# Optimization experiments

Hardware: AMD Instinct MI355X
Metric: run time of the kernel (lower is better)

The kernel has to match this reference:

```python
import jax, jax.numpy as jnp
import numpy as np

B, N, IN_FT, OUT_FT = 2, 4096, 512, 256
NEG = -9e15
EPS = 1e-12

def _prelu(x, a):
    return jnp.where(x >= 0, x, a * x)

def _normalize(x):
    n = jnp.sqrt(jnp.sum(x * x, axis=-1, keepdims=True))
    return x / jnp.maximum(n, EPS)

def _xavier(key, shape):
    fan_out, fan_in = shape
    lim = np.sqrt(6.0 / (fan_in + fan_out))
    return jax.random.uniform(key, shape, jnp.float32, -lim, lim)

def setup_inputs() -> dict:
    key = jax.random.key(0)
    ks = jax.random.split(key, 8)
    seq = jax.random.normal(ks[0], (B, N, IN_FT), jnp.float32)
    # sparse-ish random adjacency with self loops, row-normalized (typical GCN input)
    u = jax.random.uniform(ks[1], (B, N, N))
    mask = (u < 0.01).astype(jnp.float32)
    eye = jnp.eye(N, dtype=jnp.float32)[None]
    mask = jnp.maximum(mask, eye)
    adj = mask / jnp.sum(mask, axis=-1, keepdims=True)
    return {
        "seq": seq,
        "adj": adj,
        "W_fc": _xavier(ks[2], (OUT_FT, IN_FT)),
        "W_q": _xavier(ks[3], (OUT_FT, OUT_FT)),
        "W_k": _xavier(ks[4], (OUT_FT, OUT_FT)),
        "W_v1": _xavier(ks[5], (OUT_FT, OUT_FT)),
        "W_v2": _xavier(ks[6], (OUT_FT, OUT_FT)),
        "a_v": jnp.asarray(0.25, jnp.float32),    # PReLU inside to_v
        "a_act": jnp.asarray(0.25, jnp.float32),  # final PReLU self.act
        "bias": jnp.zeros((OUT_FT,), jnp.float32),
    }

def reference(seq, adj, W_fc, W_q, W_k, W_v1, W_v2, a_v, a_act, bias):
    # attn=True, training=False (dropout is identity) path of GCN.forward
    seq_fts = jnp.einsum('bnd,od->bno', seq, W_fc)            # fc (no bias)
    out = jnp.einsum('bmn,bno->bmo', adj, seq_fts)            # bmm(adj, seq_fts)
    out_q = _normalize(jnp.einsum('bno,po->bnp', out, W_q))
    out_k = _normalize(jnp.einsum('bno,po->bnp', out, W_k))
    attn_mx = jax.lax.stop_gradient(jnp.einsum('bmd,bnd->bmn', out_q, out_k))
    div_loss = jnp.mean(jnp.sum((out_q - out_k) ** 2, axis=-1))
    scores = jnp.where(adj > 0, attn_mx, NEG)
    attention = jax.nn.softmax(scores, axis=-1)               # dropout skipped (eval)
    ctx = jnp.einsum('bmn,bno->bmo', attention, out)
    h = _prelu(jnp.einsum('bno,po->bnp', ctx, W_v1), a_v)
    v = jnp.einsum('bno,po->bnp', h, W_v2)
    y = _prelu(v + bias, a_act)
    return (y, div_loss)
```

## Files before the change

kernel.cpp:

```cpp
#include <hip/hip_runtime.h>
#include <hip/hip_bf16.h>


#define NN    4096
#define ROWS  8192
#define OFT   256
#define CAP   128
#define NBLK  512
#define RPB   16
#define EPSN  1e-12f
#define MFMA(a,b,c) __builtin_amdgcn_mfma_f32_16x16x32_bf16((a),(b),(c),0,0,0)

typedef unsigned short ushort_t;
typedef unsigned char  u8;
typedef __attribute__((ext_vector_type(8))) short bf16x8;
typedef __attribute__((ext_vector_type(4))) float f32x4;
typedef __attribute__((ext_vector_type(2))) float f32x2;

#define WP_FC   0
#define WP_Q    (16384 * 8)
#define WP_K    (WP_Q + 8192 * 8)
#define WP_V1   (WP_K + 8192 * 8)
#define WP_V2   (WP_V1 + 8192 * 8)

__device__ __forceinline__ float lo_f(unsigned u) { union { unsigned i; float f; } c; c.i = u << 16;          return c.f; }
__device__ __forceinline__ float hi_f(unsigned u) { union { unsigned i; float f; } c; c.i = u & 0xFFFF0000u;  return c.f; }
__device__ __forceinline__ float bf2f(ushort_t u) { union { unsigned i; float f; } c; c.i = (unsigned)u << 16; return c.f; }
__device__ __forceinline__ ushort_t f2bf(float f) {
    union { float f; unsigned i; } c; c.f = f;
    unsigned r = c.i + 0x7FFFu + ((c.i >> 16) & 1u);
    return (ushort_t)(r >> 16);
}
__device__ __forceinline__ unsigned pack2(float a, float b) {
    return (unsigned)f2bf(a) | ((unsigned)f2bf(b) << 16);
}

template<int CTRL>
__device__ __forceinline__ float dpp_add(float x) {
    union { float f; int i; } c; c.f = x;
    int y = __builtin_amdgcn_update_dpp(c.i, c.i, CTRL, 0xF, 0xF, false);
    union { int i; float f; } r; r.i = y;
    return x + r.f;
}

__global__ __launch_bounds__(256) void k0_prep(
    const float* __restrict__ Wfc, const float* __restrict__ Wq,
    const float* __restrict__ Wk,  const float* __restrict__ Wv1,
    const float* __restrict__ Wv2, ushort_t* __restrict__ Wp)
{
    int sid = blockIdx.x * 256 + threadIdx.x;
    const float* src; int K, local; ushort_t* dst;
    if (sid < 16384) { src = Wfc; K = 512; local = sid; dst = Wp + WP_FC + (size_t)local * 8; }
    else {
        int s = sid - 16384, which = s >> 13; local = s & 8191;
        const float* ws4[4] = {Wq, Wk, Wv1, Wv2};
        src = ws4[which]; K = 256;
        dst = Wp + WP_Q + (size_t)which * 65536 + (size_t)local * 8;
    }
    int col = local & 255, k8c = local >> 8;
    const float* p = src + (size_t)col * K + k8c * 8;
    float4 x0 = *(const float4*)p, x1 = *(const float4*)(p + 4);
    uint4 o; o.x = pack2(x0.x, x0.y); o.y = pack2(x0.z, x0.w);
    o.z = pack2(x1.x, x1.y); o.w = pack2(x1.z, x1.w);
    *(uint4*)dst = o;
}

__global__ __launch_bounds__(1024, 4) void k1_extract_fc(
    const float* __restrict__ seq, const float* __restrict__ adj,
    const ushort_t* __restrict__ Wp, u8* __restrict__ regA8,
    unsigned* __restrict__ gcols, int* __restrict__ cnt)
{
    __shared__ ushort_t Astage[64 * 17 * 8];
    __shared__ ushort_t csr_c[RPB * CAP];
    __shared__ int      csr_n[RPB];

    const int tid = threadIdx.x, wave = tid >> 6, lane = tid & 63;
    const int t16 = lane & 15, kq = lane >> 4;
    const int b = blockIdx.x, r0 = b * RPB;

    {
        const float4* rowp = (const float4*)(adj + (size_t)(r0 + wave) * NN);
        float4 v[16];
#pragma unroll
        for (int t = 0; t < 16; ++t) v[t] = rowp[t * 64 + lane];
        int base = 0;
#pragma unroll
        for (int h = 0; h < 2; ++h) {
            int c = 0;
#pragma unroll
            for (int t = 0; t < 8; ++t) {
                const float4& x = v[h * 8 + t];
                c += (x.x > 0.f) + (x.y > 0.f) + (x.z > 0.f) + (x.w > 0.f);
            }
            int incl = c;
#pragma unroll
            for (int off = 1; off < 64; off <<= 1) {
                int y = __shfl_up(incl, off, 64);
                if (lane >= off) incl += y;
            }
            int p = base + incl - c;
            base += __shfl(incl, 63, 64);
#pragma unroll
            for (int t = 0; t < 8; ++t) {
                const float4& x = v[h * 8 + t];
                float f[4] = {x.x, x.y, x.z, x.w};
#pragma unroll
                for (int j = 0; j < 4; ++j)
                    if (f[j] > 0.f) {
                        if (p < CAP)
                            csr_c[wave * CAP + p] = (ushort_t)(((h * 8 + t) * 64 + lane) * 4 + j);
                        ++p;
                    }
            }
        }
        if (lane == 0) csr_n[wave] = (base < CAP) ? base : CAP;
    }
    __syncthreads();
    {
        const unsigned* cc = (const unsigned*)csr_c;
        if (tid < RPB * CAP / 2) gcols[b * (RPB * CAP / 2) + tid] = cc[tid];
        if (tid < RPB) cnt[r0 + tid] = csr_n[tid];
    }

    {
        int row = tid >> 6, seg = tid & 63;
        const float* p = seq + (size_t)(r0 + row) * 512 + seg * 8;
        float4 x0 = *(const float4*)p, x1 = *(const float4*)(p + 4);
        uint4 a;
        a.x = pack2(x0.x, x0.y); a.y = pack2(x0.z, x0.w);
        a.z = pack2(x1.x, x1.y); a.w = pack2(x1.z, x1.w);
        *(bf16x8*)(Astage + ((size_t)seg * 17 + row) * 8) = *(bf16x8*)&a;
    }
    __syncthreads();

    {
        const int col = wave * 16 + t16;
        const ushort_t* Wm = Wp + WP_FC;
        f32x4 a0 = {0.f, 0.f, 0.f, 0.f};
        for (int bch = 0; bch < 4; ++bch) {
            bf16x8 wb[4];
#pragma unroll
            for (int c2 = 0; c2 < 4; ++c2) {
                int k8c = (bch * 4 + c2) * 4 + kq;
                wb[c2] = *(const bf16x8*)(Wm + ((size_t)k8c * 256 + col) * 8);
            }
#pragma unroll
            for (int c2 = 0; c2 < 4; ++c2) {
                int c = bch * 4 + c2;
                bf16x8 af = *(const bf16x8*)(Astage + ((size_t)(c * 4 + kq) * 17 + t16) * 8);
                a0 = MFMA(af, wb[c2], a0);
            }
        }
#pragma unroll
        for (int r = 0; r < 4; ++r) {
            int t8 = __builtin_amdgcn_cvt_pk_fp8_f32(a0[r] * 16.f, 0.f, 0, false);
            regA8[(size_t)(r0 + kq * 4 + r) * OFT + col] = (u8)(t8 & 0xFF);
        }
    }
}

__global__ __launch_bounds__(1024, 4) void k2_spmm_qk(
    const u8* __restrict__ regA8, unsigned* __restrict__ KO8,
    ushort_t* __restrict__ regQ, const ushort_t* __restrict__ Wp,
    const unsigned* __restrict__ gcols, const int* __restrict__ cnt,
    float* __restrict__ part)
{
    __shared__ ushort_t Astage[32 * 17 * 8];
    __shared__ ushort_t csr_c[RPB * CAP];
    __shared__ ushort_t qn_l[RPB * OFT];
    __shared__ float    red[2][RPB][8];
    __shared__ float    dlred[16];

    const int tid = threadIdx.x, wave = tid >> 6, lane = tid & 63;
    const int t16 = lane & 15, kq = lane >> 4, grp = lane >> 4;
    const int b = blockIdx.x, r0 = b * RPB;
    const size_t batb = (size_t)(b >> 8) * 4096;

    {
        unsigned* cc = (unsigned*)csr_c;
        if (tid < RPB * CAP / 2) cc[tid] = gcols[b * (RPB * CAP / 2) + tid];
    }
    __syncthreads();

    {
        const int rl = wave;
        const int n = cnt[r0 + rl];
        const u8* gA = regA8 + batb * OFT;
        float a16[16];
#pragma unroll
        for (int j = 0; j < 16; ++j) a16[j] = 0.f;
        const int nIter = (n + 3) >> 2;
        uint4 v;
        {
            int e0 = grp; int val0 = (e0 < n);
            int col0 = csr_c[rl * CAP + (val0 ? e0 : 0)];
            v = *(const uint4*)(gA + (size_t)col0 * OFT + t16 * 16);
        }
        for (int it = 0; it < nIter; ++it) {
            uint4 vn;
            if (it + 1 < nIter) {
                int e1 = (it + 1) * 4 + grp; int val1 = (e1 < n);
                int col1 = csr_c[rl * CAP + (val1 ? e1 : 0)];
                vn = *(const uint4*)(gA + (size_t)col1 * OFT + t16 * 16);
            }
            int e = it * 4 + grp;
            if (e < n) {
                unsigned w4[4] = {v.x, v.y, v.z, v.w};
#pragma unroll
                for (int i2 = 0; i2 < 4; ++i2) {
                    f32x2 x01 = __builtin_amdgcn_cvt_pk_f32_fp8((int)w4[i2], false);
                    f32x2 x23 = __builtin_amdgcn_cvt_pk_f32_fp8((int)w4[i2], true);
                    a16[4*i2+0] += x01.x; a16[4*i2+1] += x01.y;
                    a16[4*i2+2] += x23.x; a16[4*i2+3] += x23.y;
                }
            }
            v = vn;
        }
#pragma unroll
        for (int j = 0; j < 16; ++j) {
            a16[j] += __shfl_xor(a16[j], 16, 64);
            a16[j] += __shfl_xor(a16[j], 32, 64);
        }
        float iv = 1.f / (16.f * (float)max(n, 1));
        float o0 = a16[grp*4+0]*iv, o1 = a16[grp*4+1]*iv;
        float o2 = a16[grp*4+2]*iv, o3 = a16[grp*4+3]*iv;
        int uo = 0;
        uo = __builtin_amdgcn_cvt_pk_fp8_f32(o0*16.f, o1*16.f, uo, false);
        uo = __builtin_amdgcn_cvt_pk_fp8_f32(o2*16.f, o3*16.f, uo, true);
        KO8[(size_t)(r0 + rl) * 128 + (t16 * 4 + grp) * 2 + 1] = (unsigned)uo;
        int d0 = t16 * 16 + grp * 4;
        int q8c = d0 >> 3, off = d0 & 7;
        uint2 st; st.x = pack2(o0, o1); st.y = pack2(o2, o3);
        *(uint2*)(Astage + ((size_t)q8c * 17 + rl) * 8 + off) = st;
    }
    __syncthreads();

    const int isK = wave >> 3, w8 = wave & 7;
    const ushort_t* Wm = Wp + (isK ? WP_K : WP_Q);
    f32x4 acc[2];
    acc[0] = (f32x4){0.f,0.f,0.f,0.f};
    acc[1] = (f32x4){0.f,0.f,0.f,0.f};
    for (int bch = 0; bch < 2; ++bch) {
        bf16x8 wb[2][4];
#pragma unroll
        for (int j = 0; j < 2; ++j)
#pragma unroll
            for (int c2 = 0; c2 < 4; ++c2) {
                int col = w8 * 32 + j * 16 + t16;
                int k8c = (bch * 4 + c2) * 4 + kq;
                wb[j][c2] = *(const bf16x8*)(Wm + ((size_t)k8c * 256 + col) * 8);
            }
#pragma unroll
        for (int c2 = 0; c2 < 4; ++c2) {
            int c = bch * 4 + c2;
            bf16x8 af = *(const bf16x8*)(Astage + ((size_t)(c*4 + kq) * 17 + t16) * 8);
            acc[0] = MFMA(af, wb[0][c2], acc[0]);
            acc[1] = MFMA(af, wb[1][c2], acc[1]);
        }
    }
#pragma unroll
    for (int r = 0; r < 4; ++r) {
        float s = acc[0][r]*acc[0][r] + acc[1][r]*acc[1][r];
#pragma unroll
        for (int off = 1; off < 16; off <<= 1) s += __shfl_xor(s, off, 16);
        if (t16 == 0) red[isK][kq*4 + r][w8] = s;
    }
    __syncthreads();
#pragma unroll
    for (int r = 0; r < 4; ++r) {
        int row = kq * 4 + r;
        float s = 0.f;
#pragma unroll
        for (int j = 0; j < 8; ++j) s += red[isK][row][j];
        float inv = 1.f / fmaxf(sqrtf(s), EPSN);
#pragma unroll
        for (int j = 0; j < 2; ++j) {
            int col = w8 * 32 + j * 16 + t16;
            float v = acc[j][r] * inv;
            acc[j][r] = v;
            if (isK) {
                int t8 = __builtin_amdgcn_cvt_pk_fp8_f32(v * 16.f, 0.f, 0, false);
                ((u8*)KO8)[(size_t)(r0 + row) * 512 + (col >> 2) * 8 + (col & 3)] =
                    (u8)(t8 & 0xFF);
            } else {
                ushort_t uv = f2bf(v);
                qn_l[row * OFT + col] = uv;
                regQ[(size_t)(r0 + row) * OFT + col] = uv;
            }
        }
    }
    __syncthreads();
    if (isK) {
        float dl = 0.f;
#pragma unroll
        for (int r = 0; r < 4; ++r) {
            int row = kq * 4 + r;
#pragma unroll
            for (int j = 0; j < 2; ++j) {
                int col = w8 * 32 + j * 16 + t16;
                float d = bf2f(qn_l[row * OFT + col]) - acc[j][r];
                dl += d * d;
            }
        }
#pragma unroll
        for (int off = 1; off < 64; off <<= 1) dl += __shfl_xor(dl, off, 64);
        if (lane == 0) dlred[wave] = dl;
    }
    __syncthreads();
    if (tid == 0) {
        float s = 0.f;
#pragma unroll
        for (int j = 8; j < 16; ++j) s += dlred[j];
        part[b] = s;
    }
}

__global__ __launch_bounds__(1024, 4) void k3_fused(
    const unsigned* __restrict__ KO8, const ushort_t* __restrict__ regQ,
    const unsigned* __restrict__ gcols, const int* __restrict__ cnt,
    const ushort_t* __restrict__ Wp, const float* __restrict__ a_v,
    const float* __restrict__ a_act, const float* __restrict__ biasv,
    const float* __restrict__ part, float* __restrict__ out)
{
    __shared__ ushort_t csr_c[RPB * CAP];
    __shared__ ushort_t Astage[32 * 17 * 8];
    __shared__ ushort_t Hl[32 * 17 * 8];
    __shared__ float    s8[16];

    const int tid = threadIdx.x, wave = tid >> 6, lane = tid & 63;
    const int t16 = lane & 15, kq = lane >> 4, grp = lane >> 4;
    const int b = blockIdx.x, r0 = b * RPB;
    const size_t batb = (size_t)(b >> 8) * 4096;

    if (b == 0 && tid < 512) {
        float s = part[tid];
#pragma unroll
        for (int off = 32; off; off >>= 1) s += __shfl_down(s, off, 64);
        if (lane == 0) s8[wave] = s;
    }
    __syncthreads();
    if (b == 0 && tid == 0) {
        float t = 0.f;
#pragma unroll
        for (int j = 0; j < 8; ++j) t += s8[j];
        out[(size_t)ROWS * OFT] = t * (1.f / 8192.f);
    }

    {
        unsigned* cc = (unsigned*)csr_c;
        if (tid < RPB * CAP / 2) cc[tid] = gcols[b * (RPB * CAP / 2) + tid];
    }
    __syncthreads();

    {
        const int row = r0 + wave;
        const int n = cnt[row];
        float q[16];
        {
            const ushort_t* qp = regQ + (size_t)row * OFT + t16 * 16;
            uint4 a = *(const uint4*)qp, bq = *(const uint4*)(qp + 8);
            unsigned uu[8] = {a.x, a.y, a.z, a.w, bq.x, bq.y, bq.z, bq.w};
#pragma unroll
            for (int j = 0; j < 8; ++j) { q[2*j] = lo_f(uu[j]); q[2*j+1] = hi_f(uu[j]); }
        }
        const unsigned* gKO = KO8 + batb * 128;
        float c[16];
#pragma unroll
        for (int j = 0; j < 16; ++j) c[j] = 0.f;
        float sE = 0.f;
        const int nIter = (n + 3) >> 2;
        uint4 v0, v1;
        {
            int e0 = grp; int val0 = (e0 < n);
            int col0 = csr_c[wave * CAP + (val0 ? e0 : 0)];
            const uint4* p0 = (const uint4*)(gKO + (size_t)col0 * 128 + t16 * 8);
            v0 = p0[0]; v1 = p0[1];
        }
        for (int it = 0; it < nIter; ++it) {
            uint4 n0, n1;
            if (it + 1 < nIter) {
                int e1 = (it + 1) * 4 + grp; int val1 = (e1 < n);
                int col1 = csr_c[wave * CAP + (val1 ? e1 : 0)];
                const uint4* p1 = (const uint4*)(gKO + (size_t)col1 * 128 + t16 * 8);
                n0 = p1[0]; n1 = p1[1];
            }
            int e = it * 4 + grp;
            int valid = (e < n);
            float d = 0.f;
            unsigned kw[4] = {v0.x, v0.z, v1.x, v1.z};
#pragma unroll
            for (int i2 = 0; i2 < 4; ++i2) {
                f32x2 k01 = __builtin_amdgcn_cvt_pk_f32_fp8((int)kw[i2], false);
                f32x2 k23 = __builtin_amdgcn_cvt_pk_f32_fp8((int)kw[i2], true);
                d += q[4*i2+0]*k01.x + q[4*i2+1]*k01.y + q[4*i2+2]*k23.x + q[4*i2+3]*k23.y;
            }
            d = dpp_add<0xB1>(d);
            d = dpp_add<0x4E>(d);
            d = dpp_add<0x124>(d);
            d = dpp_add<0x128>(d);
            float es = __expf(d * 0.0625f);
            es = valid ? es : 0.f;
            sE += es;
            unsigned ow[4] = {v0.y, v0.w, v1.y, v1.w};
#pragma unroll
            for (int i2 = 0; i2 < 4; ++i2) {
                f32x2 o01 = __builtin_amdgcn_cvt_pk_f32_fp8((int)ow[i2], false);
                f32x2 o23 = __builtin_amdgcn_cvt_pk_f32_fp8((int)ow[i2], true);
                c[4*i2+0] += es * o01.x; c[4*i2+1] += es * o01.y;
                c[4*i2+2] += es * o23.x; c[4*i2+3] += es * o23.y;
            }
            v0 = n0; v1 = n1;
        }
#pragma unroll
        for (int j = 0; j < 16; ++j) {
            c[j] += __shfl_xor(c[j], 16, 64);
            c[j] += __shfl_xor(c[j], 32, 64);
        }
        sE += __shfl_xor(sE, 16, 64);
        sE += __shfl_xor(sE, 32, 64);
        float inv16 = 0.0625f / sE;
        {
            int d0 = t16 * 16 + grp * 4;
            int q8c = d0 >> 3, off = d0 & 7;
            uint2 st; st.x = pack2(c[grp*4]*inv16, c[grp*4+1]*inv16);
            st.y = pack2(c[grp*4+2]*inv16, c[grp*4+3]*inv16);
            *(uint2*)(Astage + ((size_t)q8c * 17 + wave) * 8 + off) = st;
        }
    }
    __syncthreads();

    const int col = wave * 16 + t16;
    {
        const ushort_t* Wm = Wp + WP_V1;
        f32x4 h0 = {0.f,0.f,0.f,0.f};
        for (int bch = 0; bch < 2; ++bch) {
            bf16x8 wb[4];
#pragma unroll
            for (int c2 = 0; c2 < 4; ++c2) {
                int k8c = (bch * 4 + c2) * 4 + kq;
                wb[c2] = *(const bf16x8*)(Wm + ((size_t)k8c * 256 + col) * 8);
            }
#pragma unroll
            for (int c2 = 0; c2 < 4; ++c2) {
                int c = bch * 4 + c2;
                bf16x8 af = *(const bf16x8*)(Astage + ((size_t)(c*4 + kq) * 17 + t16) * 8);
                h0 = MFMA(af, wb[c2], h0);
            }
        }
        float av = *a_v;
        int q8c = col >> 3, off = col & 7;
#pragma unroll
        for (int r = 0; r < 4; ++r) {
            int row = kq * 4 + r;
            float x = h0[r]; x = (x >= 0.f) ? x : av * x;
            Hl[((size_t)q8c * 17 + row) * 8 + off] = f2bf(x);
        }
    }
    __syncthreads();

    {
        const ushort_t* Wm = Wp + WP_V2;
        f32x4 y0 = {0.f,0.f,0.f,0.f};
        for (int bch = 0; bch < 2; ++bch) {
            bf16x8 wb[4];
#pragma unroll
            for (int c2 = 0; c2 < 4; ++c2) {
                int k8c = (bch * 4 + c2) * 4 + kq;
                wb[c2] = *(const bf16x8*)(Wm + ((size_t)k8c * 256 + col) * 8);
            }
#pragma unroll
            for (int c2 = 0; c2 < 4; ++c2) {
                int c = bch * 4 + c2;
                bf16x8 af = *(const bf16x8*)(Hl + ((size_t)(c*4 + kq) * 17 + t16) * 8);
                y0 = MFMA(af, wb[c2], y0);
            }
        }
        float aa = *a_act;
        float bv = biasv[col];
#pragma unroll
        for (int r = 0; r < 4; ++r) {
            size_t row = (size_t)(r0 + kq * 4 + r);
            float x = y0[r] + bv; x = (x >= 0.f) ? x : aa * x;
            out[row * OFT + col] = x;
        }
    }
}

extern "C" void kernel_launch(void* const* d_in, const int* in_sizes, int n_in,
                              void* d_out, int out_size, void* d_ws, size_t ws_size,
                              hipStream_t stream)
{
    const float* seq   = (const float*)d_in[0];
    const float* adj   = (const float*)d_in[1];
    const float* W_fc  = (const float*)d_in[2];
    const float* W_q   = (const float*)d_in[3];
    const float* W_k   = (const float*)d_in[4];
    const float* W_v1  = (const float*)d_in[5];
    const float* W_v2  = (const float*)d_in[6];
    const float* a_v   = (const float*)d_in[7];
    const float* a_act = (const float*)d_in[8];
    const float* bias  = (const float*)d_in[9];

    char* w = (char*)d_ws;
    u8*       regA8 = (u8*)w;
    unsigned* KO8   = (unsigned*)(w + (4u  << 20));
    ushort_t* regQ  = (ushort_t*)(w + (12u << 20));
    unsigned* gcols = (unsigned*)(w + (16u << 20));
    int*      cnt   = (int*)(w + (20u << 20));
    float*    part  = (float*)(w + (20u << 20) + 32768);
    ushort_t* Wp    = (ushort_t*)(w + (21u << 20));

    k0_prep<<<192, 256, 0, stream>>>(W_fc, W_q, W_k, W_v1, W_v2, Wp);
    k1_extract_fc<<<NBLK, 1024, 0, stream>>>(seq, adj, Wp, regA8, gcols, cnt);
    k2_spmm_qk<<<NBLK, 1024, 0, stream>>>(regA8, KO8, regQ, Wp, gcols, cnt, part);
    k3_fused<<<NBLK, 1024, 0, stream>>>(KO8, regQ, gcols, cnt, Wp,
                                        a_v, a_act, bias, part, (float*)d_out);
}
```

Measured before the change: 276.3 us.

## Fold W_k into query side so attention gathers only aggregated features

Rewrites q·k as (q·W_k)·out scaled by each neighbor's inverse K-norm. k2 now computes h = q_norm·W_k (using a transposed bf16 copy of W_k) and stores per-row K inverse norms, and it no longer writes normalized K. k3 then gathers a single 8-bit vector per neighbor, serving both the score dot product and the context accumulation. This halves the per-edge gather bytes in the attention loop, at the cost of an extra small MFMA pass in k2, an extra prep section, and a per-edge lookup of the inverse norm.

```diff
diff --git a/kernel.cpp b/kernel.cpp
--- a/kernel.cpp
+++ b/kernel.cpp
@@ -8,6 +8,7 @@
 #define CAP   128
 #define NBLK  512
 #define RPB   16
+#define QLS   264
 #define EPSN  1e-12f
 #define MFMA(a,b,c) __builtin_amdgcn_mfma_f32_16x16x32_bf16((a),(b),(c),0,0,0)
 
@@ -22,6 +23,7 @@
 #define WP_K    (WP_Q + 8192 * 8)
 #define WP_V1   (WP_K + 8192 * 8)
 #define WP_V2   (WP_V1 + 8192 * 8)
+#define WP_KT   (WP_V2 + 8192 * 8)
 
 __device__ __forceinline__ float lo_f(unsigned u) { union { unsigned i; float f; } c; c.i = u << 16;          return c.f; }
 __device__ __forceinline__ float hi_f(unsigned u) { union { unsigned i; float f; } c; c.i = u & 0xFFFF0000u;  return c.f; }
@@ -49,6 +51,16 @@
     const float* __restrict__ Wv2, ushort_t* __restrict__ Wp)
 {
     int sid = blockIdx.x * 256 + threadIdx.x;
+    if (sid >= 49152) {
+        int t = sid - 49152;
+        int o = t & 255, p8 = t >> 8;
+        ushort_t tmp[8];
+#pragma unroll
+        for (int i = 0; i < 8; ++i)
+            tmp[i] = f2bf(Wk[(size_t)(p8 * 8 + i) * 256 + o]);
+        *(bf16x8*)(Wp + WP_KT + (size_t)t * 8) = *(bf16x8*)tmp;
+        return;
+    }
     const float* src; int K, local; ushort_t* dst;
     if (sid < 16384) { src = Wfc; K = 512; local = sid; dst = Wp + WP_FC + (size_t)local * 8; }
     else {
@@ -161,13 +173,13 @@
 
 __global__ __launch_bounds__(1024, 4) void k2_spmm_qk(
     const u8* __restrict__ regA8, unsigned* __restrict__ KO8,
-    ushort_t* __restrict__ regQ, const ushort_t* __restrict__ Wp,
+    ushort_t* __restrict__ regH, const ushort_t* __restrict__ Wp,
     const unsigned* __restrict__ gcols, const int* __restrict__ cnt,
-    float* __restrict__ part)
+    float* __restrict__ part, float* __restrict__ invnk_g)
 {
     __shared__ ushort_t Astage[32 * 17 * 8];
     __shared__ ushort_t csr_c[RPB * CAP];
-    __shared__ ushort_t qn_l[RPB * OFT];
+    __shared__ ushort_t qn_l[RPB * QLS];
     __shared__ float    red[2][RPB][8];
     __shared__ float    dlred[16];
 
@@ -227,7 +239,7 @@
         int uo = 0;
         uo = __builtin_amdgcn_cvt_pk_fp8_f32(o0*16.f, o1*16.f, uo, false);
         uo = __builtin_amdgcn_cvt_pk_fp8_f32(o2*16.f, o3*16.f, uo, true);
-        KO8[(size_t)(r0 + rl) * 128 + (t16 * 4 + grp) * 2 + 1] = (unsigned)uo;
+        KO8[(size_t)(r0 + rl) * 64 + (t16 * 4 + grp)] = (unsigned)uo;
         int d0 = t16 * 16 + grp * 4;
         int q8c = d0 >> 3, off = d0 & 7;
         uint2 st; st.x = pack2(o0, o1); st.y = pack2(o2, o3);
@@ -273,20 +285,13 @@
 #pragma unroll
         for (int j = 0; j < 8; ++j) s += red[isK][row][j];
         float inv = 1.f / fmaxf(sqrtf(s), EPSN);
+        if (isK && w8 == 0 && t16 == 0) invnk_g[r0 + row] = inv;
 #pragma unroll
         for (int j = 0; j < 2; ++j) {
             int col = w8 * 32 + j * 16 + t16;
             float v = acc[j][r] * inv;
             acc[j][r] = v;
-            if (isK) {
-                int t8 = __builtin_amdgcn_cvt_pk_fp8_f32(v * 16.f, 0.f, 0, false);
-                ((u8*)KO8)[(size_t)(r0 + row) * 512 + (col >> 2) * 8 + (col & 3)] =
-                    (u8)(t8 & 0xFF);
-            } else {
-                ushort_t uv = f2bf(v);
-                qn_l[row * OFT + col] = uv;
-                regQ[(size_t)(r0 + row) * OFT + col] = uv;
-            }
+            if (!isK) qn_l[row * QLS + col] = f2bf(v);
         }
     }
     __syncthreads();
@@ -298,7 +303,7 @@
 #pragma unroll
             for (int j = 0; j < 2; ++j) {
                 int col = w8 * 32 + j * 16 + t16;
-                float d = bf2f(qn_l[row * OFT + col]) - acc[j][r];
+                float d = bf2f(qn_l[row * QLS + col]) - acc[j][r];
                 dl += d * d;
             }
         }
@@ -307,6 +312,31 @@
         if (lane == 0) dlred[wave] = dl;
     }
     __syncthreads();
+
+    {
+        const ushort_t* WmT = Wp + WP_KT;
+        const int colh = wave * 16 + t16;
+        f32x4 h0 = {0.f, 0.f, 0.f, 0.f};
+        for (int bch = 0; bch < 2; ++bch) {
+            bf16x8 wb[4];
+#pragma unroll
+            for (int c2 = 0; c2 < 4; ++c2) {
+                int k8c = (bch * 4 + c2) * 4 + kq;
+                wb[c2] = *(const bf16x8*)(WmT + ((size_t)k8c * 256 + colh) * 8);
+            }
+#pragma unroll
+            for (int c2 = 0; c2 < 4; ++c2) {
+                int k8c = (bch * 4 + c2) * 4 + kq;
+                bf16x8 af = *(const bf16x8*)(qn_l + (size_t)t16 * QLS + k8c * 8);
+                h0 = MFMA(af, wb[c2], h0);
+            }
+        }
+#pragma unroll
+        for (int r = 0; r < 4; ++r) {
+            int row = kq * 4 + r;
+            regH[(size_t)(r0 + row) * OFT + colh] = f2bf(h0[r]);
+        }
+    }
     if (tid == 0) {
         float s = 0.f;
 #pragma unroll
@@ -316,13 +346,15 @@
 }
 
 __global__ __launch_bounds__(1024, 4) void k3_fused(
-    const unsigned* __restrict__ KO8, const ushort_t* __restrict__ regQ,
+    const unsigned* __restrict__ KO8, const ushort_t* __restrict__ regH,
     const unsigned* __restrict__ gcols, const int* __restrict__ cnt,
     const ushort_t* __restrict__ Wp, const float* __restrict__ a_v,
     const float* __restrict__ a_act, const float* __restrict__ biasv,
-    const float* __restrict__ part, float* __restrict__ out)
+    const float* __restrict__ part, const float* __restrict__ invnk_g,
+    float* __restrict__ out)
 {
     __shared__ ushort_t csr_c[RPB * CAP];
+    __shared__ float    invl[RPB][CAP];
     __shared__ ushort_t Astage[32 * 17 * 8];
     __shared__ ushort_t Hl[32 * 17 * 8];
     __shared__ float    s8[16];
@@ -355,61 +387,66 @@
     {
         const int row = r0 + wave;
         const int n = cnt[row];
+#pragma unroll
+        for (int s = 0; s < 2; ++s) {
+            int e = lane + s * 64;
+            if (e < n) {
+                int col = csr_c[wave * CAP + e];
+                invl[wave][e] = invnk_g[batb + col] * 0.0625f;
+            }
+        }
         float q[16];
         {
-            const ushort_t* qp = regQ + (size_t)row * OFT + t16 * 16;
+            const ushort_t* qp = regH + (size_t)row * OFT + t16 * 16;
             uint4 a = *(const uint4*)qp, bq = *(const uint4*)(qp + 8);
             unsigned uu[8] = {a.x, a.y, a.z, a.w, bq.x, bq.y, bq.z, bq.w};
 #pragma unroll
             for (int j = 0; j < 8; ++j) { q[2*j] = lo_f(uu[j]); q[2*j+1] = hi_f(uu[j]); }
         }
-        const unsigned* gKO = KO8 + batb * 128;
+        const unsigned* gKO = KO8 + batb * 64;
         float c[16];
 #pragma unroll
         for (int j = 0; j < 16; ++j) c[j] = 0.f;
         float sE = 0.f;
         const int nIter = (n + 3) >> 2;
-        uint4 v0, v1;
+        uint4 v;
         {
             int e0 = grp; int val0 = (e0 < n);
             int col0 = csr_c[wave * CAP + (val0 ? e0 : 0)];
-            const uint4* p0 = (const uint4*)(gKO + (size_t)col0 * 128 + t16 * 8);
-            v0 = p0[0]; v1 = p0[1];
+            v = *(const uint4*)(gKO + (size_t)col0 * 64 + t16 * 4);
         }
         for (int it = 0; it < nIter; ++it) {
-            uint4 n0, n1;
+            uint4 vn;
             if (it + 1 < nIter) {
                 int e1 = (it + 1) * 4 + grp; int val1 = (e1 < n);
                 int col1 = csr_c[wave * CAP + (val1 ? e1 : 0)];
-                const uint4* p1 = (const uint4*)(gKO + (size_t)col1 * 128 + t16 * 8);
-                n0 = p1[0]; n1 = p1[1];
+                vn = *(const uint4*)(gKO + (size_t)col1 * 64 + t16 * 4);
             }
             int e = it * 4 + grp;
             int valid = (e < n);
+            float o[16];
+            unsigned w4[4] = {v.x, v.y, v.z, v.w};
+#pragma unroll
+            for (int i2 = 0; i2 < 4; ++i2) {
+                f32x2 x01 = __builtin_amdgcn_cvt_pk_f32_fp8((int)w4[i2], false);
+                f32x2 x23 = __builtin_amdgcn_cvt_pk_f32_fp8((int)w4[i2], true);
+                o[4*i2+0] = x01.x; o[4*i2+1] = x01.y;
+                o[4*i2+2] = x23.x; o[4*i2+3] = x23.y;
+            }
             float d = 0.f;
-            unsigned kw[4] = {v0.x, v0.z, v1.x, v1.z};
-#pragma unroll
-            for (int i2 = 0; i2 < 4; ++i2) {
-                f32x2 k01 = __builtin_amdgcn_cvt_pk_f32_fp8((int)kw[i2], false);
-                f32x2 k23 = __builtin_amdgcn_cvt_pk_f32_fp8((int)kw[i2], true);
-                d += q[4*i2+0]*k01.x + q[4*i2+1]*k01.y + q[4*i2+2]*k23.x + q[4*i2+3]*k23.y;
-            }
+#pragma unroll
+            for (int j = 0; j < 16; ++j) d += q[j] * o[j];
             d = dpp_add<0xB1>(d);
             d = dpp_add<0x4E>(d);
             d = dpp_add<0x124>(d);
             d = dpp_add<0x128>(d);
-            float es = __expf(d * 0.0625f);
+            float iv16v = invl[wave][valid ? e : 0];
+            float es = __expf(d * iv16v);
             es = valid ? es : 0.f;
             sE += es;
-            unsigned ow[4] = {v0.y, v0.w, v1.y, v1.w};
-#pragma unroll
-            for (int i2 = 0; i2 < 4; ++i2) {
-                f32x2 o01 = __builtin_amdgcn_cvt_pk_f32_fp8((int)ow[i2], false);
-                f32x2 o23 = __builtin_amdgcn_cvt_pk_f32_fp8((int)ow[i2], true);
-                c[4*i2+0] += es * o01.x; c[4*i2+1] += es * o01.y;
-                c[4*i2+2] += es * o23.x; c[4*i2+3] += es * o23.y;
-            }
-            v0 = n0; v1 = n1;
+#pragma unroll
+            for (int j = 0; j < 16; ++j) c[j] += es * o[j];
+            v = vn;
         }
 #pragma unroll
         for (int j = 0; j < 16; ++j) {
@@ -504,15 +541,18 @@
     char* w = (char*)d_ws;
     u8*       regA8 = (u8*)w;
     unsigned* KO8   = (unsigned*)(w + (4u  << 20));
-    ushort_t* regQ  = (ushort_t*)(w + (12u << 20));
+    ushort_t* regH  = (ushort_t*)(w + (12u << 20));
     unsigned* gcols = (unsigned*)(w + (16u << 20));
     int*      cnt   = (int*)(w + (20u << 20));
     float*    part  = (float*)(w + (20u << 20) + 32768);
+    float*    invnk = (float*)(w + (20u << 20) + 65536);
     ushort_t* Wp    = (ushort_t*)(w + (21u << 20));
 
-    k0_prep<<<192, 256, 0, stream>>>(W_fc, W_q, W_k, W_v1, W_v2, Wp);
+    k0_prep<<<224, 256, 0, stream>>>(W_fc, W_q, W_k, W_v1, W_v2, Wp);
     k1_extract_fc<<<NBLK, 1024, 0, stream>>>(seq, adj, Wp, regA8, gcols, cnt);
-    k2_spmm_qk<<<NBLK, 1024, 0, stream>>>(regA8, KO8, regQ, Wp, gcols, cnt, part);
-    k3_fused<<<NBLK, 1024, 0, stream>>>(KO8, regQ, gcols, cnt, Wp,
-                                        a_v, a_act, bias, part, (float*)d_out);
-}
+    k2_spmm_qk<<<NBLK, 1024, 0, stream>>>(regA8, KO8, regH, Wp, gcols, cnt,
+                                          part, invnk);
+    k3_fused<<<NBLK, 1024, 0, stream>>>(KO8, regH, gcols, cnt, Wp,
+                                        a_v, a_act, bias, part, invnk,
+                                        (float*)d_out);
+}
```

After: 274.7 us. About the same (-0.6%).
